# Kernel optimization log

Hardware: AMD Instinct MI355X
Metric: run time of the kernel (lower is better)

Reference implementation:

```python
import jax, jax.numpy as jnp
import numpy as np

EPS = 1e-6

def _ln(x, w, b):
    mu = jnp.mean(x, axis=-1, keepdims=True)
    var = jnp.mean((x - mu) ** 2, axis=-1, keepdims=True)
    return (x - mu) * jax.lax.rsqrt(var + EPS) * w + b

def setup_inputs() -> dict:
    B, N, C, H, P = 64, 197, 768, 12, 20
    Dh = C // H
    Dff = 4 * C
    key = jax.random.key(0)
    ks = jax.random.split(key, 16)
    s = 0.02
    return {
        "x": jax.random.normal(ks[0], (B, N, C), jnp.float32),
        "prompt": jax.random.normal(ks[1], (B, P, 2, H, Dh), jnp.float32),
        "ln1_w": jnp.ones((C,), jnp.float32),
        "ln1_b": jnp.zeros((C,), jnp.float32),
        "qkv_w": jax.random.normal(ks[2], (3 * C, C), jnp.float32) * s,
        "qkv_b": jnp.zeros((3 * C,), jnp.float32),
        "proj_w": jax.random.normal(ks[3], (C, C), jnp.float32) * s,
        "proj_b": jnp.zeros((C,), jnp.float32),
        "ln2_w": jnp.ones((C,), jnp.float32),
        "ln2_b": jnp.zeros((C,), jnp.float32),
        "fc1_w": jax.random.normal(ks[4], (Dff, C), jnp.float32) * s,
        "fc1_b": jnp.zeros((Dff,), jnp.float32),
        "fc2_w": jax.random.normal(ks[5], (C, Dff), jnp.float32) * s,
        "fc2_b": jnp.zeros((C,), jnp.float32),
    }

def reference(x, prompt, ln1_w, ln1_b, qkv_w, qkv_b, proj_w, proj_b,
              ln2_w, ln2_b, fc1_w, fc1_b, fc2_w, fc2_b):
    B, N, C = x.shape
    H = 12
    Dh = C // H
    scale = Dh ** -0.5

    # --- attention branch ---
    h = _ln(x, ln1_w, ln1_b)
    qkv = (h @ qkv_w.T + qkv_b).reshape(B, N, 3, H, Dh)
    qkv = jnp.transpose(qkv, (2, 0, 3, 1, 4))  # [3, B, H, N, Dh]
    q, k, v = qkv[0], qkv[1], qkv[2]

    # prompt: [B, P, 2, H, Dh] -> [2, B, H, P, Dh]
    pr = jnp.transpose(prompt, (2, 0, 3, 1, 4))
    k = jnp.concatenate([pr[0], k], axis=2)  # [B, H, P+N, Dh]
    v = jnp.concatenate([pr[1], v], axis=2)

    attn = jnp.einsum('bhnd,bhmd->bhnm', q, k) * scale
    attn = jax.nn.softmax(attn, axis=-1)
    o = jnp.einsum('bhnm,bhmd->bhnd', attn, v)
    o = jnp.transpose(o, (0, 2, 1, 3)).reshape(B, N, C)
    o = o @ proj_w.T + proj_b
    x = x + o

    # --- mlp branch ---
    h2 = _ln(x, ln2_w, ln2_b)
    m = jax.nn.gelu(h2 @ fc1_w.T + fc1_b, approximate=False)
    m = m @ fc2_w.T + fc2_b
    return x + m
```

## Files before the change

kernel.cpp:

```cpp
#include <hip/hip_runtime.h>
#include <hip/hip_bf16.h>

typedef __attribute__((ext_vector_type(4))) float f32x4;
typedef __attribute__((ext_vector_type(8))) __bf16 bfv8;
typedef __attribute__((ext_vector_type(8))) short sv8;
typedef __attribute__((ext_vector_type(4))) unsigned short usv4;


static __device__ __forceinline__ f32x4 mfma16(sv8 a, sv8 b, f32x4 c) {
    return __builtin_amdgcn_mfma_f32_16x16x32_bf16(
        __builtin_bit_cast(bfv8, a), __builtin_bit_cast(bfv8, b), c, 0, 0, 0);
}

static __device__ __forceinline__ unsigned short f2bf(float f) {
    union { float f; unsigned int u; } v; v.f = f;
    unsigned int u = v.u;
    return (unsigned short)((u + 0x7FFFu + ((u >> 16) & 1u)) >> 16);
}

static __device__ __forceinline__ void gld16(void* lds, const void* g) {
    __builtin_amdgcn_global_load_lds(
        (const __attribute__((address_space(1))) unsigned int*)g,
        (__attribute__((address_space(3))) unsigned int*)lds, 16, 0, 0);
}


__global__ void cvt_bf16_kernel(const float* __restrict__ in,
                                unsigned short* __restrict__ out, int n4) {
    int i = blockIdx.x * 256 + threadIdx.x;
    if (i >= n4) return;
    float4 f = reinterpret_cast<const float4*>(in)[i];
    usv4 o = { f2bf(f.x), f2bf(f.y), f2bf(f.z), f2bf(f.w) };
    reinterpret_cast<usv4*>(out)[i] = o;
}


__global__ void ln_kernel(const float* __restrict__ x, const float* __restrict__ w,
                          const float* __restrict__ b, unsigned short* __restrict__ out) {
    const int row = blockIdx.x;
    const int t = threadIdx.x;
    const float* xr = x + (size_t)row * 768;
    float v[3];
    float s = 0.f, ss = 0.f;
#pragma unroll
    for (int i = 0; i < 3; ++i) {
        v[i] = xr[t + i * 256];
        s += v[i]; ss += v[i] * v[i];
    }
#pragma unroll
    for (int o = 32; o; o >>= 1) { s += __shfl_xor(s, o); ss += __shfl_xor(ss, o); }
    __shared__ float red[8];
    if ((t & 63) == 0) { red[t >> 6] = s; red[4 + (t >> 6)] = ss; }
    __syncthreads();
    float S = red[0] + red[1] + red[2] + red[3];
    float SS = red[4] + red[5] + red[6] + red[7];
    float mu = S * (1.0f / 768.0f);
    float var = SS * (1.0f / 768.0f) - mu * mu;
    float rstd = rsqrtf(var + 1e-6f);
#pragma unroll
    for (int i = 0; i < 3; ++i) {
        int c = t + i * 256;
        out[(size_t)row * 768 + c] = f2bf((v[i] - mu) * rstd * w[c] + b[c]);
    }
}


__global__ void prompt_kernel(const float* __restrict__ pr,
                              unsigned short* __restrict__ k_out,
                              unsigned short* __restrict__ v_out) {
    int i = blockIdx.x * 256 + threadIdx.x;
    if (i >= 64 * 20 * 12 * 64) return;
    int d = i & 63;
    int t = i >> 6;
    int h = t % 12;
    int t2 = t / 12;
    int p = t2 % 20;
    int b = t2 / 20;
    size_t src = ((((size_t)b * 20 + p) * 2 + 0) * 12 + h) * 64 + d;
    float kv = pr[src];
    float vv = pr[src + 12 * 64];
    k_out[(((size_t)(b * 12 + h) * 224 + p) << 6) + d] = f2bf(kv);
    v_out[((size_t)(b * 12 + h) * 64 + d) * 224 + p] = f2bf(vv);
}


#define EPI_QKV 0
#define EPI_RES 1
#define EPI_GELU 2

template <int EPI>
__global__ void gemm_bf16(const unsigned short* __restrict__ A,
                          const unsigned short* __restrict__ W,
                          const float* __restrict__ bias,
                          const float* __restrict__ resid,
                          void* __restrict__ out0,
                          unsigned short* __restrict__ q_out,
                          unsigned short* __restrict__ k_out,
                          unsigned short* __restrict__ v_out,
                          int M, int N, int K) {
    __shared__ __align__(16) unsigned short As[128 * 32];
    __shared__ __align__(16) unsigned short Bs[128 * 32];
    const int tid = threadIdx.x;
    const int lane = tid & 63;
    const int wave = tid >> 6;
    const int wm = wave >> 1, wn = wave & 1;
    const int bm = blockIdx.x, bn = blockIdx.y;
    const int rl = lane & 15, kg = lane >> 4;

    f32x4 acc[4][4];
#pragma unroll
    for (int i = 0; i < 4; ++i)
#pragma unroll
        for (int j = 0; j < 4; ++j) acc[i][j] = f32x4{0.f, 0.f, 0.f, 0.f};

    const int nk = K >> 5;
    for (int kt = 0; kt < nk; ++kt) {
        const int k0 = kt << 5;
#pragma unroll
        for (int i = 0; i < 2; ++i) {
            const int c = i * 256 + tid;
            const int row = c >> 2, sl = c & 3;
            const int ss = sl ^ ((row >> 1) & 3);
            int ar = bm * 128 + row; ar = ar < M ? ar : M - 1;
            gld16(&As[c * 8], &A[(size_t)ar * K + k0 + ss * 8]);
            gld16(&Bs[c * 8], &W[(size_t)(bn * 128 + row) * K + k0 + ss * 8]);
        }
        __syncthreads();
        sv8 af[4], bfr[4];
#pragma unroll
        for (int f = 0; f < 4; ++f) {
            const int ra = wm * 64 + f * 16 + rl;
            af[f] = *reinterpret_cast<const sv8*>(&As[ra * 32 + (kg ^ ((ra >> 1) & 3)) * 8]);
            const int rb = wn * 64 + f * 16 + rl;
            bfr[f] = *reinterpret_cast<const sv8*>(&Bs[rb * 32 + (kg ^ ((rb >> 1) & 3)) * 8]);
        }
#pragma unroll
        for (int i = 0; i < 4; ++i)
#pragma unroll
            for (int j = 0; j < 4; ++j) acc[i][j] = mfma16(af[i], bfr[j], acc[i][j]);
        __syncthreads();
    }

#pragma unroll
    for (int i = 0; i < 4; ++i) {
        const int m0 = bm * 128 + wm * 64 + i * 16 + kg * 4;
#pragma unroll
        for (int j = 0; j < 4; ++j) {
            const int ncol = bn * 128 + wn * 64 + j * 16 + rl;
            const float bia = bias[ncol];
#pragma unroll
            for (int r = 0; r < 4; ++r) {
                const int m = m0 + r;
                if (m >= M) continue;
                float vv = acc[i][j][r] + bia;
                if constexpr (EPI == EPI_QKV) {
                    int b = m / 197, nn = m - b * 197;
                    int which = ncol / 768;
                    int rr = ncol - which * 768;
                    int h = rr >> 6;
                    int d = ncol & 63;
                    if (which == 0)
                        q_out[(((size_t)(b * 12 + h) * 197 + nn) << 6) + d] = f2bf(vv);
                    else if (which == 1)
                        k_out[(((size_t)(b * 12 + h) * 224 + 20 + nn) << 6) + d] = f2bf(vv);
                    else
                        v_out[((size_t)(b * 12 + h) * 64 + d) * 224 + 20 + nn] = f2bf(vv);
                } else if constexpr (EPI == EPI_RES) {
                    ((float*)out0)[(size_t)m * N + ncol] = vv + resid[(size_t)m * N + ncol];
                } else {
                    float g = 0.5f * vv * (1.0f + erff(vv * 0.70710678118f));
                    ((unsigned short*)out0)[(size_t)m * N + ncol] = f2bf(g);
                }
            }
        }
    }
}


__global__ void attn_kernel(const unsigned short* __restrict__ Qg,
                            const unsigned short* __restrict__ Kg,
                            const unsigned short* __restrict__ Vtg,
                            unsigned short* __restrict__ obuf) {
    __shared__ __align__(16) unsigned short sKS[14848];
    __shared__ __align__(16) unsigned short sV[64 * 232];
    const int tid = threadIdx.x;
    const int lane = tid & 63;
    const int wave = tid >> 6;
    const int rl = lane & 15, kg = lane >> 4;
    const int qt = blockIdx.x, h = blockIdx.y, b = blockIdx.z;
    const size_t bh = (size_t)b * 12 + h;
    const size_t qbase = bh * 197 * 64;
    const size_t kbase = bh * 224 * 64;
    const size_t vbase = bh * 64 * 224;

    int qrow = qt * 64 + wave * 16 + rl;
    if (qrow > 196) qrow = 196;
    sv8 qf[2];
#pragma unroll
    for (int ks = 0; ks < 2; ++ks)
        qf[ks] = *reinterpret_cast<const sv8*>(&Qg[qbase + (size_t)qrow * 64 + ks * 32 + kg * 8]);

#pragma unroll
    for (int i = 0; i < 7; ++i) {
        const int c = i * 256 + tid;
        const int key = c >> 3, sl = c & 7;
        const int ssl = sl ^ (key & 7);
        gld16(&sKS[c * 8], &Kg[kbase + key * 64 + ssl * 8]);
    }
#pragma unroll
    for (int i = 0; i < 7; ++i) {
        const int c = i * 256 + tid;
        const int d = c / 28, sl = c - d * 28;
        sv8 val = *reinterpret_cast<const sv8*>(&Vtg[vbase + d * 224 + sl * 8]);
        *reinterpret_cast<sv8*>(&sV[d * 232 + sl * 8]) = val;
    }
    __syncthreads();

    f32x4 sacc[14];
#pragma unroll
    for (int f = 0; f < 14; ++f) sacc[f] = f32x4{0.f, 0.f, 0.f, 0.f};
#pragma unroll
    for (int f = 0; f < 14; ++f) {
        const int key = f * 16 + rl;
#pragma unroll
        for (int ks = 0; ks < 2; ++ks) {
            const int sl = (ks * 4 + kg) ^ (key & 7);
            sv8 kf = *reinterpret_cast<const sv8*>(&sKS[key * 64 + sl * 8]);
            sacc[f] = mfma16(qf[ks], kf, sacc[f]);
        }
    }

    float mx[4] = {-1e30f, -1e30f, -1e30f, -1e30f};
#pragma unroll
    for (int f = 0; f < 14; ++f) {
        const int col = f * 16 + rl;
#pragma unroll
        for (int r = 0; r < 4; ++r) {
            float s = sacc[f][r] * 0.125f;
            if (col >= 217) s = -1e30f;
            sacc[f][r] = s;
            mx[r] = fmaxf(mx[r], s);
        }
    }
#pragma unroll
    for (int o = 1; o < 16; o <<= 1)
#pragma unroll
        for (int r = 0; r < 4; ++r) mx[r] = fmaxf(mx[r], __shfl_xor(mx[r], o));
    float sm[4] = {0.f, 0.f, 0.f, 0.f};
#pragma unroll
    for (int f = 0; f < 14; ++f)
#pragma unroll
        for (int r = 0; r < 4; ++r) {
            float e = __expf(sacc[f][r] - mx[r]);
            sacc[f][r] = e;
            sm[r] += e;
        }
#pragma unroll
    for (int o = 1; o < 16; o <<= 1)
#pragma unroll
        for (int r = 0; r < 4; ++r) sm[r] += __shfl_xor(sm[r], o);
    float inv[4];
#pragma unroll
    for (int r = 0; r < 4; ++r) inv[r] = 1.0f / sm[r];

    __syncthreads();
    unsigned short* Sl = sKS;
#pragma unroll
    for (int f = 0; f < 14; ++f)
#pragma unroll
        for (int r = 0; r < 4; ++r)
            Sl[(wave * 16 + kg * 4 + r) * 232 + f * 16 + rl] = f2bf(sacc[f][r] * inv[r]);
    __syncthreads();

    f32x4 oacc[4];
#pragma unroll
    for (int fd = 0; fd < 4; ++fd) oacc[fd] = f32x4{0.f, 0.f, 0.f, 0.f};
#pragma unroll
    for (int ks = 0; ks < 7; ++ks) {
        sv8 pf = *reinterpret_cast<const sv8*>(&Sl[(wave * 16 + rl) * 232 + ks * 32 + kg * 8]);
#pragma unroll
        for (int fd = 0; fd < 4; ++fd) {
            sv8 vf = *reinterpret_cast<const sv8*>(&sV[(fd * 16 + rl) * 232 + ks * 32 + kg * 8]);
            oacc[fd] = mfma16(pf, vf, oacc[fd]);
        }
    }

#pragma unroll
    for (int fd = 0; fd < 4; ++fd)
#pragma unroll
        for (int r = 0; r < 4; ++r) {
            const int q = qt * 64 + wave * 16 + kg * 4 + r;
            if (q < 197)
                obuf[((size_t)b * 197 + q) * 768 + h * 64 + fd * 16 + rl] = f2bf(oacc[fd][r]);
        }
}


extern "C" void kernel_launch(void* const* d_in, const int* in_sizes, int n_in,
                              void* d_out, int out_size, void* d_ws, size_t ws_size,
                              hipStream_t stream) {
    const float* x      = (const float*)d_in[0];
    const float* prompt = (const float*)d_in[1];
    const float* ln1_w  = (const float*)d_in[2];
    const float* ln1_b  = (const float*)d_in[3];
    const float* qkv_w  = (const float*)d_in[4];
    const float* qkv_b  = (const float*)d_in[5];
    const float* proj_w = (const float*)d_in[6];
    const float* proj_b = (const float*)d_in[7];
    const float* ln2_w  = (const float*)d_in[8];
    const float* ln2_b  = (const float*)d_in[9];
    const float* fc1_w  = (const float*)d_in[10];
    const float* fc1_b  = (const float*)d_in[11];
    const float* fc2_w  = (const float*)d_in[12];
    const float* fc2_b  = (const float*)d_in[13];

    char* ws = (char*)d_ws;
    size_t off = 0;
    auto bump = [&](size_t bytes) {
        char* p = ws + off;
        off += (bytes + 255) & ~(size_t)255;
        return p;
    };
    unsigned short* qkvw  = (unsigned short*)bump(2304UL * 768 * 2);
    unsigned short* projw = (unsigned short*)bump(768UL * 768 * 2);
    unsigned short* fc1w  = (unsigned short*)bump(3072UL * 768 * 2);
    unsigned short* fc2w  = (unsigned short*)bump(768UL * 3072 * 2);
    unsigned short* h2    = (unsigned short*)bump(12608UL * 768 * 2);
    float* xmid           = (float*)bump(12608UL * 768 * 4);
    char* pool = ws + off;
    unsigned short* h1   = (unsigned short*)(pool);
    unsigned short* Qg   = (unsigned short*)(pool + 19365888UL);
    unsigned short* Kg   = (unsigned short*)(pool + 38731776UL);
    unsigned short* Vtg  = (unsigned short*)(pool + 60751872UL);
    unsigned short* obuf = (unsigned short*)(pool + 82771968UL);
    unsigned short* mbuf = (unsigned short*)(pool);

    cvt_bf16_kernel<<<(2304 * 768 / 4 + 255) / 256, 256, 0, stream>>>(qkv_w, qkvw, 2304 * 768 / 4);
    cvt_bf16_kernel<<<(768 * 768 / 4 + 255) / 256, 256, 0, stream>>>(proj_w, projw, 768 * 768 / 4);
    cvt_bf16_kernel<<<(3072 * 768 / 4 + 255) / 256, 256, 0, stream>>>(fc1_w, fc1w, 3072 * 768 / 4);
    cvt_bf16_kernel<<<(768 * 3072 / 4 + 255) / 256, 256, 0, stream>>>(fc2_w, fc2w, 768 * 3072 / 4);

    ln_kernel<<<12608, 256, 0, stream>>>(x, ln1_w, ln1_b, h1);
    prompt_kernel<<<983040 / 256, 256, 0, stream>>>(prompt, Kg, Vtg);

    gemm_bf16<EPI_QKV><<<dim3(99, 18), 256, 0, stream>>>(
        h1, qkvw, qkv_b, nullptr, nullptr, Qg, Kg, Vtg, 12608, 2304, 768);

    attn_kernel<<<dim3(4, 12, 64), 256, 0, stream>>>(Qg, Kg, Vtg, obuf);

    gemm_bf16<EPI_RES><<<dim3(99, 6), 256, 0, stream>>>(
        obuf, projw, proj_b, x, xmid, nullptr, nullptr, nullptr, 12608, 768, 768);

    ln_kernel<<<12608, 256, 0, stream>>>(xmid, ln2_w, ln2_b, h2);

    gemm_bf16<EPI_GELU><<<dim3(99, 24), 256, 0, stream>>>(
        h2, fc1w, fc1_b, nullptr, mbuf, nullptr, nullptr, nullptr, 12608, 3072, 768);

    gemm_bf16<EPI_RES><<<dim3(99, 6), 256, 0, stream>>>(
        mbuf, fc2w, fc2_b, xmid, (float*)d_out, nullptr, nullptr, nullptr, 12608, 768, 3072);
}
```

Measured before the change: 498.1 us.

## Replace GEMM with 256x256 double-buffered 8-wave pipelined kernel with XCD remap

Replaces the 128x128, 4-wave single-buffered GEMM with a 256x256-tile, 8-wave kernel using a double-buffered 64-wide K stage. Global-to-LDS loads for the next tiles are interleaved with MFMA quarters under explicit barriers, waitcnts and setprio, so memory traffic overlaps compute. A 1D grid is remapped so consecutive tiles land on the same XCD for L2 reuse. Larger tiles cut redundant operand loads, but the small N GEMMs (768) now launch only 150 blocks, which may underfill the device. Register pressure is also higher.

```diff
diff --git a/kernel.cpp b/kernel.cpp
--- a/kernel.cpp
+++ b/kernel.cpp
@@ -23,6 +23,10 @@
         (const __attribute__((address_space(1))) unsigned int*)g,
         (__attribute__((address_space(3))) unsigned int*)lds, 16, 0, 0);
 }
+
+#define BAR() __builtin_amdgcn_s_barrier()
+#define SCHED() __builtin_amdgcn_sched_barrier(0)
+#define LGKM0() asm volatile("s_waitcnt lgkmcnt(0)" ::: "memory")
 
 
 __global__ void cvt_bf16_kernel(const float* __restrict__ in,
@@ -89,75 +93,156 @@
 #define EPI_GELU 2
 
 template <int EPI>
-__global__ void gemm_bf16(const unsigned short* __restrict__ A,
-                          const unsigned short* __restrict__ W,
-                          const float* __restrict__ bias,
-                          const float* __restrict__ resid,
-                          void* __restrict__ out0,
-                          unsigned short* __restrict__ q_out,
-                          unsigned short* __restrict__ k_out,
-                          unsigned short* __restrict__ v_out,
-                          int M, int N, int K) {
-    __shared__ __align__(16) unsigned short As[128 * 32];
-    __shared__ __align__(16) unsigned short Bs[128 * 32];
+__launch_bounds__(512, 2)
+__global__ void gemm8(const unsigned short* __restrict__ A,
+                      const unsigned short* __restrict__ W,
+                      const float* __restrict__ bias,
+                      const float* __restrict__ resid,
+                      void* __restrict__ out0,
+                      unsigned short* __restrict__ q_out,
+                      unsigned short* __restrict__ k_out,
+                      unsigned short* __restrict__ v_out,
+                      int M, int N, int K, int NB) {
+    __shared__ __align__(16) unsigned short lds[2][2][256][64];
     const int tid = threadIdx.x;
     const int lane = tid & 63;
-    const int wave = tid >> 6;
-    const int wm = wave >> 1, wn = wave & 1;
-    const int bm = blockIdx.x, bn = blockIdx.y;
+    const int wid = tid >> 6;
+    const int wm = wid >> 2, wn = wid & 3;
     const int rl = lane & 15, kg = lane >> 4;
 
-    f32x4 acc[4][4];
-#pragma unroll
-    for (int i = 0; i < 4; ++i)
-#pragma unroll
-        for (int j = 0; j < 4; ++j) acc[i][j] = f32x4{0.f, 0.f, 0.f, 0.f};
-
-    const int nk = K >> 5;
-    for (int kt = 0; kt < nk; ++kt) {
-        const int k0 = kt << 5;
-#pragma unroll
-        for (int i = 0; i < 2; ++i) {
-            const int c = i * 256 + tid;
-            const int row = c >> 2, sl = c & 3;
-            const int ss = sl ^ ((row >> 1) & 3);
-            int ar = bm * 128 + row; ar = ar < M ? ar : M - 1;
-            gld16(&As[c * 8], &A[(size_t)ar * K + k0 + ss * 8]);
-            gld16(&Bs[c * 8], &W[(size_t)(bn * 128 + row) * K + k0 + ss * 8]);
-        }
-        __syncthreads();
-        sv8 af[4], bfr[4];
-#pragma unroll
-        for (int f = 0; f < 4; ++f) {
-            const int ra = wm * 64 + f * 16 + rl;
-            af[f] = *reinterpret_cast<const sv8*>(&As[ra * 32 + (kg ^ ((ra >> 1) & 3)) * 8]);
-            const int rb = wn * 64 + f * 16 + rl;
-            bfr[f] = *reinterpret_cast<const sv8*>(&Bs[rb * 32 + (kg ^ ((rb >> 1) & 3)) * 8]);
-        }
-#pragma unroll
-        for (int i = 0; i < 4; ++i)
-#pragma unroll
-            for (int j = 0; j < 4; ++j) acc[i][j] = mfma16(af[i], bfr[j], acc[i][j]);
-        __syncthreads();
-    }
-
-#pragma unroll
-    for (int i = 0; i < 4; ++i) {
-        const int m0 = bm * 128 + wm * 64 + i * 16 + kg * 4;
-#pragma unroll
-        for (int j = 0; j < 4; ++j) {
-            const int ncol = bn * 128 + wn * 64 + j * 16 + rl;
+    const int nwg = gridDim.x;
+    const int orig = blockIdx.x;
+    const int xcd = orig & 7;
+    const int qq = nwg >> 3, rr = nwg & 7;
+    const int wg = (xcd < rr ? xcd * (qq + 1) : rr * (qq + 1) + (xcd - rr) * qq) + (orig >> 3);
+    const int bm = wg / NB, bn = wg - bm * NB;
+
+    const int NT = K >> 6;
+
+    auto stage = [&](int t, int X, int h) {
+        const unsigned short* src = (X == 0) ? A : W;
+        const int pb = ((X == 0) ? bm : bn) * 256 + h * 128;
+        unsigned short* dst = &lds[t & 1][X][h * 128][0];
+#pragma unroll
+        for (int j = 0; j < 2; ++j) {
+            const int c = j * 512 + tid;
+            const int rw = c >> 3, sl = c & 7;
+            const int ssl = sl ^ (rw & 7);
+            int rg = pb + rw;
+            if (X == 0 && rg >= M) rg = M - 1;
+            gld16(dst + c * 8, src + (size_t)rg * K + t * 64 + ssl * 8);
+        }
+    };
+
+    f32x4 acc[8][4];
+#pragma unroll
+    for (int m = 0; m < 8; ++m)
+#pragma unroll
+        for (int n = 0; n < 4; ++n) acc[m][n] = f32x4{0.f, 0.f, 0.f, 0.f};
+
+    stage(0, 0, 0); stage(0, 0, 1); stage(0, 1, 0); stage(0, 1, 1);
+    stage(1, 0, 0); stage(1, 0, 1);
+    asm volatile("s_waitcnt vmcnt(4)" ::: "memory");
+    BAR();
+
+    for (int t = 0; t < NT; ++t) {
+        const int buf = t & 1;
+        sv8 af[8][2], bf[4][2];
+#pragma unroll
+        for (int m = 0; m < 4; ++m)
+#pragma unroll
+            for (int ks = 0; ks < 2; ++ks)
+                af[m][ks] = *(const sv8*)&lds[buf][0][wm * 128 + m * 16 + rl][(((ks << 2) | kg) ^ (rl & 7)) << 3];
+#pragma unroll
+        for (int n = 0; n < 2; ++n)
+#pragma unroll
+            for (int ks = 0; ks < 2; ++ks)
+                bf[n][ks] = *(const sv8*)&lds[buf][1][wn * 64 + n * 16 + rl][(((ks << 2) | kg) ^ (rl & 7)) << 3];
+        if (t + 1 < NT) stage(t + 1, 1, 0);
+        BAR();
+        LGKM0(); SCHED();
+        __builtin_amdgcn_s_setprio(1);
+#pragma unroll
+        for (int m = 0; m < 4; ++m)
+#pragma unroll
+            for (int n = 0; n < 2; ++n)
+#pragma unroll
+                for (int ks = 0; ks < 2; ++ks)
+                    acc[m][n] = mfma16(af[m][ks], bf[n][ks], acc[m][n]);
+        __builtin_amdgcn_s_setprio(0); SCHED();
+        BAR();
+#pragma unroll
+        for (int m = 4; m < 8; ++m)
+#pragma unroll
+            for (int ks = 0; ks < 2; ++ks)
+                af[m][ks] = *(const sv8*)&lds[buf][0][wm * 128 + m * 16 + rl][(((ks << 2) | kg) ^ (rl & 7)) << 3];
+        if (t + 1 < NT) stage(t + 1, 1, 1);
+        BAR();
+        LGKM0(); SCHED();
+        __builtin_amdgcn_s_setprio(1);
+#pragma unroll
+        for (int m = 4; m < 8; ++m)
+#pragma unroll
+            for (int n = 0; n < 2; ++n)
+#pragma unroll
+                for (int ks = 0; ks < 2; ++ks)
+                    acc[m][n] = mfma16(af[m][ks], bf[n][ks], acc[m][n]);
+        __builtin_amdgcn_s_setprio(0); SCHED();
+        BAR();
+#pragma unroll
+        for (int n = 2; n < 4; ++n)
+#pragma unroll
+            for (int ks = 0; ks < 2; ++ks)
+                bf[n][ks] = *(const sv8*)&lds[buf][1][wn * 64 + n * 16 + rl][(((ks << 2) | kg) ^ (rl & 7)) << 3];
+        if (t + 2 < NT) stage(t + 2, 0, 0);
+        BAR();
+        LGKM0(); SCHED();
+        __builtin_amdgcn_s_setprio(1);
+#pragma unroll
+        for (int m = 0; m < 4; ++m)
+#pragma unroll
+            for (int n = 2; n < 4; ++n)
+#pragma unroll
+                for (int ks = 0; ks < 2; ++ks)
+                    acc[m][n] = mfma16(af[m][ks], bf[n][ks], acc[m][n]);
+        __builtin_amdgcn_s_setprio(0); SCHED();
+        BAR();
+        if (t + 2 < NT) {
+            stage(t + 2, 0, 1);
+            asm volatile("s_waitcnt vmcnt(4)" ::: "memory");
+        } else if (t + 1 < NT) {
+            asm volatile("s_waitcnt vmcnt(0)" ::: "memory");
+        }
+        BAR();
+        __builtin_amdgcn_s_setprio(1);
+#pragma unroll
+        for (int m = 4; m < 8; ++m)
+#pragma unroll
+            for (int n = 2; n < 4; ++n)
+#pragma unroll
+                for (int ks = 0; ks < 2; ++ks)
+                    acc[m][n] = mfma16(af[m][ks], bf[n][ks], acc[m][n]);
+        __builtin_amdgcn_s_setprio(0); SCHED();
+        BAR();
+    }
+
+#pragma unroll
+    for (int m = 0; m < 8; ++m) {
+        const int gm0 = bm * 256 + wm * 128 + m * 16 + kg * 4;
+#pragma unroll
+        for (int n = 0; n < 4; ++n) {
+            const int ncol = bn * 256 + wn * 64 + n * 16 + rl;
             const float bia = bias[ncol];
 #pragma unroll
             for (int r = 0; r < 4; ++r) {
-                const int m = m0 + r;
-                if (m >= M) continue;
-                float vv = acc[i][j][r] + bia;
+                const int mm = gm0 + r;
+                if (mm >= M) continue;
+                float vv = acc[m][n][r] + bia;
                 if constexpr (EPI == EPI_QKV) {
-                    int b = m / 197, nn = m - b * 197;
+                    int b = mm / 197, nn = mm - b * 197;
                     int which = ncol / 768;
-                    int rr = ncol - which * 768;
-                    int h = rr >> 6;
+                    int rc = ncol - which * 768;
+                    int h = rc >> 6;
                     int d = ncol & 63;
                     if (which == 0)
                         q_out[(((size_t)(b * 12 + h) * 197 + nn) << 6) + d] = f2bf(vv);
@@ -166,10 +251,10 @@
                     else
                         v_out[((size_t)(b * 12 + h) * 64 + d) * 224 + 20 + nn] = f2bf(vv);
                 } else if constexpr (EPI == EPI_RES) {
-                    ((float*)out0)[(size_t)m * N + ncol] = vv + resid[(size_t)m * N + ncol];
+                    ((float*)out0)[(size_t)mm * N + ncol] = vv + resid[(size_t)mm * N + ncol];
                 } else {
                     float g = 0.5f * vv * (1.0f + erff(vv * 0.70710678118f));
-                    ((unsigned short*)out0)[(size_t)m * N + ncol] = f2bf(g);
+                    ((unsigned short*)out0)[(size_t)mm * N + ncol] = f2bf(g);
                 }
             }
         }
@@ -343,19 +428,19 @@
     ln_kernel<<<12608, 256, 0, stream>>>(x, ln1_w, ln1_b, h1);
     prompt_kernel<<<983040 / 256, 256, 0, stream>>>(prompt, Kg, Vtg);
 
-    gemm_bf16<EPI_QKV><<<dim3(99, 18), 256, 0, stream>>>(
-        h1, qkvw, qkv_b, nullptr, nullptr, Qg, Kg, Vtg, 12608, 2304, 768);
+    gemm8<EPI_QKV><<<50 * 9, 512, 0, stream>>>(
+        h1, qkvw, qkv_b, nullptr, nullptr, Qg, Kg, Vtg, 12608, 2304, 768, 9);
 
     attn_kernel<<<dim3(4, 12, 64), 256, 0, stream>>>(Qg, Kg, Vtg, obuf);
 
-    gemm_bf16<EPI_RES><<<dim3(99, 6), 256, 0, stream>>>(
-        obuf, projw, proj_b, x, xmid, nullptr, nullptr, nullptr, 12608, 768, 768);
+    gemm8<EPI_RES><<<50 * 3, 512, 0, stream>>>(
+        obuf, projw, proj_b, x, xmid, nullptr, nullptr, nullptr, 12608, 768, 768, 3);
 
     ln_kernel<<<12608, 256, 0, stream>>>(xmid, ln2_w, ln2_b, h2);
 
-    gemm_bf16<EPI_GELU><<<dim3(99, 24), 256, 0, stream>>>(
-        h2, fc1w, fc1_b, nullptr, mbuf, nullptr, nullptr, nullptr, 12608, 3072, 768);
-
-    gemm_bf16<EPI_RES><<<dim3(99, 6), 256, 0, stream>>>(
-        mbuf, fc2w, fc2_b, xmid, (float*)d_out, nullptr, nullptr, nullptr, 12608, 768, 3072);
-}
+    gemm8<EPI_GELU><<<50 * 12, 512, 0, stream>>>(
+        h2, fc1w, fc1_b, nullptr, mbuf, nullptr, nullptr, nullptr, 12608, 3072, 768, 12);
+
+    gemm8<EPI_RES><<<50 * 3, 512, 0, stream>>>(
+        mbuf, fc2w, fc2_b, xmid, (float*)d_out, nullptr, nullptr, nullptr, 12608, 768, 3072, 3);
+}
```

Result: slower. 676.9 us (+35.9%).
